# Kernel tuning notes

Measured on AMD Instinct MI355X. Metric: run time of the kernel, lower is better.

## Reference

```python
import jax, jax.numpy as jnp
import numpy as np

B, D_IN, D_H, D_OUT = 1024, 1024, 4096, 1024
SPARSITY = 0.5  # fraction of weights KEPT (top-k)


def setup_inputs() -> dict:
    key = jax.random.key(0)
    ks = jax.random.split(key, 13)
    def kaiming(k, shape):
        fan_in = shape[-1] if len(shape) > 1 else shape[0]
        bound = 1.0 / np.sqrt(fan_in)
        return jax.random.uniform(k, shape, jnp.float32, -bound, bound)
    inp = {
        "x":   jax.random.normal(ks[0], (B, D_IN), jnp.float32),
        "W1":  kaiming(ks[1], (D_H, D_IN)),
        "b1":  kaiming(ks[2], (D_H,)),
        "W2":  kaiming(ks[3], (D_H, D_H)),
        "b2":  kaiming(ks[4], (D_H,)),
        "W3":  kaiming(ks[5], (D_OUT, D_H)),
        "b3":  kaiming(ks[6], (D_OUT,)),
        # scores: kaiming-uniform for weights, N(0, 0.01) for biases (as in Mask.__init__)
        "sW1": kaiming(ks[7], (D_H, D_IN)),
        "sb1": 0.01 * jax.random.normal(ks[8], (D_H,), jnp.float32),
        "sW2": kaiming(ks[9], (D_H, D_H)),
        "sb2": 0.01 * jax.random.normal(ks[10], (D_H,), jnp.float32),
        "sW3": kaiming(ks[11], (D_OUT, D_H)),
        "sb3": 0.01 * jax.random.normal(ks[12], (D_OUT,), jnp.float32),
    }
    return inp


def _global_masks(scores):
    """Single fused global top-k threshold mask (replaces O(P) redundant sorts).
    Bottom (1-SPARSITY) fraction (by value rank) -> 0, top SPARSITY fraction -> 1."""
    flat = jnp.concatenate([s.ravel() for s in scores])
    n = flat.shape[0]
    j = int((1.0 - SPARSITY) * n)  # number of zeroed entries
    idx = jnp.argsort(flat)
    bin_mask = jnp.zeros((n,), flat.dtype).at[idx[j:]].set(1.0)
    # straight-through: d(mask)/d(score) = 1 (GetSubnet_global.backward returns g)
    st_mask = bin_mask + flat - jax.lax.stop_gradient(flat)
    sizes = [int(np.prod(s.shape)) for s in scores]
    offs = np.concatenate([[0], np.cumsum(sizes)])
    return [st_mask[offs[i]:offs[i + 1]].reshape(scores[i].shape)
            for i in range(len(scores))]


def reference(x, W1, b1, W2, b2, W3, b3, sW1, sb1, sW2, sb2, sW3, sb3):
    masks = _global_masks([sW1, sb1, sW2, sb2, sW3, sb3])
    mW1, mb1, mW2, mb2, mW3, mb3 = masks
    # masked params, then MLP forward (torch Linear: y = x @ W.T + b)
    h = jax.nn.relu(x @ (W1 * mW1).T + b1 * mb1)
    h = jax.nn.relu(h @ (W2 * mW2).T + b2 * mb2)
    return h @ (W3 * mW3).T + b3 * mb3
```

## Files before the change

### kernel.cpp

```cpp
#include <hip/hip_runtime.h>
#include <hip/hip_bf16.h>
#include <stdint.h>


typedef __bf16 bf16_t;
typedef __bf16 bf16x4 __attribute__((ext_vector_type(4)));
typedef __bf16 bf16x8 __attribute__((ext_vector_type(8)));
typedef float  f32x4  __attribute__((ext_vector_type(4)));

using gvoid = const __attribute__((address_space(1))) void;
using svoid = __attribute__((address_space(3))) void;

#define O1 4194304L
#define O2 4198400L
#define O3 20975616L
#define O4 20979712L
#define O5 25174016L
#define N_TOT 25175040L
#define J_RANK 12587520u
#define CAND_CAP 4096

#define WS_HIST 0u
#define WS_RES  32768u
#define WS_CNT  32784u
#define WS_CAND 32800u
#define WS_W1B  131072u
#define WS_B1F  8519680u
#define WS_W2B  8536064u
#define WS_B2F  42090496u
#define WS_W3B  42106880u
#define WS_B3F  50495488u
#define WS_H1F  50511872u
#define WS_H2F  58900480u
#define WS_FAST_END 67289088ull
#define WS_H1   131072u
#define WS_H2   8519680u

#define SWZ(row, chunk) ((((chunk) + ((row) >> 1)) & 3))

__device__ __forceinline__ unsigned int mono32(float f) {
    unsigned int u = __float_as_uint(f);
    return (u & 0x80000000u) ? ~u : (u | 0x80000000u);
}

__global__ __launch_bounds__(256) void zero_kernel(unsigned int* p, int n) {
    int i = blockIdx.x * 256 + threadIdx.x;
    if (i < n) p[i] = 0u;
}

__global__ __launch_bounds__(256) void cvt_x_kernel(const float* __restrict__ x,
                                                    bf16_t* __restrict__ xb, int n8) {
    int i = blockIdx.x * 256 + threadIdx.x;
    if (i < n8) {
        const float4 a = *(const float4*)(x + (size_t)i * 8);
        const float4 b = *(const float4*)(x + (size_t)i * 8 + 4);
        bf16x8 r;
        r[0] = (__bf16)a.x; r[1] = (__bf16)a.y; r[2] = (__bf16)a.z; r[3] = (__bf16)a.w;
        r[4] = (__bf16)b.x; r[5] = (__bf16)b.y; r[6] = (__bf16)b.z; r[7] = (__bf16)b.w;
        *(bf16x8*)(xb + (size_t)i * 8) = r;
    }
}

__device__ __forceinline__ void seg_lookup(long e,
    const float* s0, const float* s1, const float* s2,
    const float* s3, const float* s4, const float* s5,
    const float** sp, long* off) {
    if (e < O1)      { *sp = s0; *off = e; }
    else if (e < O2) { *sp = s1; *off = e - O1; }
    else if (e < O3) { *sp = s2; *off = e - O2; }
    else if (e < O4) { *sp = s3; *off = e - O3; }
    else if (e < O5) { *sp = s4; *off = e - O4; }
    else             { *sp = s5; *off = e - O5; }
}

__global__ __launch_bounds__(256) void hist_kernel(
    const float* s0, const float* s1, const float* s2,
    const float* s3, const float* s4, const float* s5,
    unsigned int* hist) {
    __shared__ unsigned int lh[8192];
    for (int i = threadIdx.x; i < 8192; i += 256) lh[i] = 0u;
    __syncthreads();
    const long ng = N_TOT / 4;
    for (long g = (long)blockIdx.x * 256 + threadIdx.x; g < ng;
         g += (long)gridDim.x * 256) {
        long e = g * 4;
        const float* sp; long o;
        seg_lookup(e, s0, s1, s2, s3, s4, s5, &sp, &o);
        float4 v = *(const float4*)(sp + o);
        atomicAdd(&lh[mono32(v.x) >> 19], 1u);
        atomicAdd(&lh[mono32(v.y) >> 19], 1u);
        atomicAdd(&lh[mono32(v.z) >> 19], 1u);
        atomicAdd(&lh[mono32(v.w) >> 19], 1u);
    }
    __syncthreads();
    for (int i = threadIdx.x; i < 8192; i += 256) {
        unsigned int c = lh[i];
        if (c) atomicAdd(&hist[i], c);
    }
}

__global__ __launch_bounds__(256) void select_kernel(const unsigned int* hist,
                                                     unsigned int* res) {
    __shared__ unsigned int part[256];
    int tid = threadIdx.x;
    unsigned int s = 0;
    for (int b = tid * 32; b < tid * 32 + 32; ++b) s += hist[b];
    part[tid] = s;
    __syncthreads();
    if (tid == 0) {
        unsigned int acc = 0;
        for (int i = 0; i < 256; ++i) { unsigned int v = part[i]; part[i] = acc; acc += v; }
    }
    __syncthreads();
    unsigned int acc = part[tid];
    for (int b = tid * 32; b < tid * 32 + 32; ++b) {
        unsigned int h = hist[b];
        if (acc <= J_RANK && J_RANK < acc + h) {
            res[0] = (unsigned int)b;
            res[1] = acc;
            res[2] = J_RANK - acc;
        }
        acc += h;
    }
}

__global__ __launch_bounds__(256) void mask_apply_fast(
    const float* s0, const float* s1, const float* s2,
    const float* s3, const float* s4, const float* s5,
    const float* w0, const float* w1, const float* w2,
    const float* w3, const float* w4, const float* w5,
    bf16_t* W1b, float* b1f, bf16_t* W2b, float* b2f, bf16_t* W3b, float* b3f,
    const unsigned int* res, unsigned int* cand_cnt, unsigned long long* cand) {
    const unsigned int C = res[0];
    const long ng = N_TOT / 4;
    for (long g = (long)blockIdx.x * 256 + threadIdx.x; g < ng;
         g += (long)gridDim.x * 256) {
        long e = g * 4;
        const float* sp; long o;
        seg_lookup(e, s0, s1, s2, s3, s4, s5, &sp, &o);
        const float* wp;
        if (e < O1)      wp = w0;
        else if (e < O2) wp = w1;
        else if (e < O3) wp = w2;
        else if (e < O4) wp = w3;
        else if (e < O5) wp = w4;
        else             wp = w5;
        float4 sv = *(const float4*)(sp + o);
        float4 wv = *(const float4*)(wp + o);
#define PROC(comp, ci)                                                         \
        { unsigned int key = mono32(sv.comp); unsigned int kb = key >> 19;     \
          if (kb < C) wv.comp = 0.f;                                           \
          else if (kb == C) {                                                  \
              unsigned int slot = atomicAdd(cand_cnt, 1u);                     \
              if (slot < CAND_CAP)                                             \
                  cand[slot] = (((unsigned long long)key) << 32) |             \
                               (unsigned long long)(unsigned int)(e + ci);     \
          } }
        PROC(x, 0) PROC(y, 1) PROC(z, 2) PROC(w, 3)
#undef PROC
        if (e < O1) {
            bf16x4 b; b[0]=(__bf16)wv.x; b[1]=(__bf16)wv.y; b[2]=(__bf16)wv.z; b[3]=(__bf16)wv.w;
            *(bf16x4*)(W1b + o) = b;
        } else if (e < O2) {
            *(float4*)(b1f + o) = wv;
        } else if (e < O3) {
            bf16x4 b; b[0]=(__bf16)wv.x; b[1]=(__bf16)wv.y; b[2]=(__bf16)wv.z; b[3]=(__bf16)wv.w;
            *(bf16x4*)(W2b + o) = b;
        } else if (e < O4) {
            *(float4*)(b2f + o) = wv;
        } else if (e < O5) {
            bf16x4 b; b[0]=(__bf16)wv.x; b[1]=(__bf16)wv.y; b[2]=(__bf16)wv.z; b[3]=(__bf16)wv.w;
            *(bf16x4*)(W3b + o) = b;
        } else {
            *(float4*)(b3f + o) = wv;
        }
    }
}

__global__ __launch_bounds__(256) void finalize_fast(
    const unsigned int* res, const unsigned int* cand_cnt,
    const unsigned long long* cand,
    bf16_t* W1b, float* b1f, bf16_t* W2b, float* b2f, bf16_t* W3b, float* b3f) {
    __shared__ unsigned long long buf[CAND_CAP];
    int tid = threadIdx.x;
    unsigned int cnt = *cand_cnt; if (cnt > CAND_CAP) cnt = CAND_CAP;
    unsigned int need = res[2];   if (need > cnt) need = cnt;
    for (int i = tid; i < (int)cnt; i += 256) buf[i] = cand[i];
    __syncthreads();
    for (int i = tid; i < (int)cnt; i += 256) {
        unsigned long long me = buf[i];
        unsigned int rank = 0;
        for (unsigned int j = 0; j < cnt; ++j) rank += (buf[j] < me);
        if (rank < need) {
            long idx = (long)(unsigned int)(me & 0xFFFFFFFFu);
            if (idx < O1)      W1b[idx] = (__bf16)0.f;
            else if (idx < O2) b1f[idx - O1] = 0.f;
            else if (idx < O3) W2b[idx - O2] = (__bf16)0.f;
            else if (idx < O4) b2f[idx - O3] = 0.f;
            else if (idx < O5) W3b[idx - O4] = (__bf16)0.f;
            else               b3f[idx - O5] = 0.f;
        }
    }
}

__global__ __launch_bounds__(256) void mask_apply_kernel(
    const float* s0, const float* s1, const float* s2,
    const float* s3, const float* s4, const float* s5,
    float* w0, float* w1, float* w2, float* w3, float* w4, float* w5,
    const unsigned int* res, unsigned int* cand_cnt, unsigned long long* cand) {
    const unsigned int C = res[0];
    const long ng = N_TOT / 4;
    for (long g = (long)blockIdx.x * 256 + threadIdx.x; g < ng;
         g += (long)gridDim.x * 256) {
        long e = g * 4;
        const float* sp; long o;
        seg_lookup(e, s0, s1, s2, s3, s4, s5, &sp, &o);
        float* wp;
        if (e < O1)      wp = w0;
        else if (e < O2) wp = w1;
        else if (e < O3) wp = w2;
        else if (e < O4) wp = w3;
        else if (e < O5) wp = w4;
        else             wp = w5;
        float4 sv = *(const float4*)(sp + o);
        float4 wv = *(float4*)(wp + o);
#define PROC(comp, ci)                                                         \
        { unsigned int key = mono32(sv.comp); unsigned int kb = key >> 19;     \
          if (kb < C) wv.comp = 0.f;                                           \
          else if (kb == C) {                                                  \
              unsigned int slot = atomicAdd(cand_cnt, 1u);                     \
              if (slot < CAND_CAP)                                             \
                  cand[slot] = (((unsigned long long)key) << 32) |             \
                               (unsigned long long)(unsigned int)(e + ci);     \
          } }
        PROC(x, 0) PROC(y, 1) PROC(z, 2) PROC(w, 3)
#undef PROC
        *(float4*)(wp + o) = wv;
    }
}

__global__ __launch_bounds__(256) void finalize_kernel(
    const unsigned int* res, const unsigned int* cand_cnt,
    const unsigned long long* cand,
    float* w0, float* w1, float* w2, float* w3, float* w4, float* w5) {
    __shared__ unsigned long long buf[CAND_CAP];
    int tid = threadIdx.x;
    unsigned int cnt = *cand_cnt; if (cnt > CAND_CAP) cnt = CAND_CAP;
    unsigned int need = res[2];   if (need > cnt) need = cnt;
    for (int i = tid; i < (int)cnt; i += 256) buf[i] = cand[i];
    __syncthreads();
    for (int i = tid; i < (int)cnt; i += 256) {
        unsigned long long me = buf[i];
        unsigned int rank = 0;
        for (unsigned int j = 0; j < cnt; ++j) rank += (buf[j] < me);
        if (rank < need) {
            long idx = (long)(unsigned int)(me & 0xFFFFFFFFu);
            if (idx < O1)      w0[idx] = 0.f;
            else if (idx < O2) w1[idx - O1] = 0.f;
            else if (idx < O3) w2[idx - O2] = 0.f;
            else if (idx < O4) w3[idx - O3] = 0.f;
            else if (idx < O5) w4[idx - O4] = 0.f;
            else               w5[idx - O5] = 0.f;
        }
    }
}

__device__ __forceinline__ bf16x8 load8(const float* p) {
    float4 a = *(const float4*)p;
    float4 b = *(const float4*)(p + 4);
    bf16x8 r;
    r[0] = (__bf16)a.x; r[1] = (__bf16)a.y; r[2] = (__bf16)a.z; r[3] = (__bf16)a.w;
    r[4] = (__bf16)b.x; r[5] = (__bf16)b.y; r[6] = (__bf16)b.z; r[7] = (__bf16)b.w;
    return r;
}
__device__ __forceinline__ bf16x8 load8(const bf16_t* p) {
    return *(const bf16x8*)p;
}

template <int BM, int BN, bool RELU, typename TA, typename TB, typename TC>
__global__ __launch_bounds__(256) void gemm_bt(
    const TA* __restrict__ A, const TB* __restrict__ B,
    const float* __restrict__ bias, TC* __restrict__ C,
    int M, int N, int K) {
    constexpr int BK = 32;
    constexpr int WM = BM / 2, WN = BN / 2;
    constexpr int TM = WM / 16, TN = WN / 16;
    constexpr int CA = (BM * BK) / 8;
    constexpr int CB = (BN * BK) / 8;
    __shared__ __align__(16) bf16_t As[BM * BK];
    __shared__ __align__(16) bf16_t Bs[BN * BK];

    const int tid = threadIdx.x;
    const int w = tid >> 6, lane = tid & 63;
    const int quad = lane >> 4, l16 = lane & 15;
    const int wm = (w >> 1) * WM, wn = (w & 1) * WN;
    const int rowBase = blockIdx.y * BM;
    const int colBase = blockIdx.x * BN;

    f32x4 acc[TM][TN] = {};

    const TA* Ab = A + (size_t)rowBase * K;
    const TB* Bb = B + (size_t)colBase * K;

    for (int k0 = 0; k0 < K; k0 += BK) {
        __syncthreads();
#pragma unroll
        for (int c0 = 0; c0 < CA; c0 += 256) {
            int c = c0 + tid;
            int row = c >> 2, kc = c & 3;
            *(bf16x8*)&As[row * BK + SWZ(row, kc) * 8] =
                load8(Ab + (size_t)row * K + k0 + kc * 8);
        }
#pragma unroll
        for (int c0 = 0; c0 < CB; c0 += 256) {
            int c = c0 + tid;
            int row = c >> 2, kc = c & 3;
            *(bf16x8*)&Bs[row * BK + SWZ(row, kc) * 8] =
                load8(Bb + (size_t)row * K + k0 + kc * 8);
        }
        __syncthreads();
        bf16x8 af[TM], bfr[TN];
#pragma unroll
        for (int i = 0; i < TM; ++i) {
            int r = wm + i * 16 + l16;
            af[i] = *(const bf16x8*)&As[r * BK + SWZ(r, quad) * 8];
        }
#pragma unroll
        for (int j = 0; j < TN; ++j) {
            int r = wn + j * 16 + l16;
            bfr[j] = *(const bf16x8*)&Bs[r * BK + SWZ(r, quad) * 8];
        }
#pragma unroll
        for (int i = 0; i < TM; ++i)
#pragma unroll
            for (int j = 0; j < TN; ++j)
                acc[i][j] = __builtin_amdgcn_mfma_f32_16x16x32_bf16(
                    af[i], bfr[j], acc[i][j], 0, 0, 0);
    }

#pragma unroll
    for (int i = 0; i < TM; ++i) {
#pragma unroll
        for (int j = 0; j < TN; ++j) {
            int col = colBase + wn + j * 16 + l16;
            float bv = bias[col];
#pragma unroll
            for (int r = 0; r < 4; ++r) {
                int rowg = rowBase + wm + i * 16 + quad * 4 + r;
                float v = acc[i][j][r] + bv;
                if (RELU) v = v > 0.f ? v : 0.f;
                if constexpr (sizeof(TC) == 4)
                    C[(size_t)rowg * N + col] = v;
                else
                    C[(size_t)rowg * N + col] = (bf16_t)v;
            }
        }
    }
}

template <bool RELU, int SPLITK, typename TC>
__global__ __launch_bounds__(256) void gemm_pipe(
    const bf16_t* __restrict__ A, const bf16_t* __restrict__ B,
    const float* __restrict__ bias, TC* __restrict__ C,
    int M, int N, int K) {
    constexpr int BM = 128, BN = 128, BK = 32;
    constexpr int TM = 4, TN = 4;
    constexpr int CA = (BM * BK) / 8;
    constexpr int CB = (BN * BK) / 8;
    static_assert(CA == 512 && CB == 512, "vmcnt immediates assume 4 loads/thread/step");
    __shared__ __align__(16) bf16_t As[3][BM * BK];
    __shared__ __align__(16) bf16_t Bs[3][BN * BK];

    const int tid = threadIdx.x;
    const int w = tid >> 6, lane = tid & 63;
    const int quad = lane >> 4, l16 = lane & 15;
    const int wm = (w >> 1) * 64, wn = (w & 1) * 64;
    const int rowBase = blockIdx.y * BM;
    const int colBase = blockIdx.x * BN;

    f32x4 acc[TM][TN] = {};

    const bf16_t* Ab = A + (size_t)rowBase * K;
    const bf16_t* Bb = B + (size_t)colBase * K;

    const int kPart = K / SPLITK;
    const int kBeg = (SPLITK > 1) ? (int)blockIdx.z * kPart : 0;
    const int nt = kPart / BK;

    const int rA0 = tid >> 2,        lA0 = (((tid) & 3) - (rA0 >> 1)) & 3;
    const int cH  = tid + 256;
    const int rA1 = cH >> 2,         lA1 = ((cH & 3) - (rA1 >> 1)) & 3;
    const bf16_t* aSrc0 = Ab + (size_t)rA0 * K + lA0 * 8;
    const bf16_t* aSrc1 = Ab + (size_t)rA1 * K + lA1 * 8;
    const bf16_t* bSrc0 = Bb + (size_t)rA0 * K + lA0 * 8;
    const bf16_t* bSrc1 = Bb + (size_t)rA1 * K + lA1 * 8;

    auto stage = [&](int buf, int k0) {
        __builtin_amdgcn_global_load_lds((gvoid*)(aSrc0 + k0),
            (svoid*)(As[buf] + (size_t)tid * 8), 16, 0, 0);
        __builtin_amdgcn_global_load_lds((gvoid*)(aSrc1 + k0),
            (svoid*)(As[buf] + (size_t)cH * 8), 16, 0, 0);
        __builtin_amdgcn_global_load_lds((gvoid*)(bSrc0 + k0),
            (svoid*)(Bs[buf] + (size_t)tid * 8), 16, 0, 0);
        __builtin_amdgcn_global_load_lds((gvoid*)(bSrc1 + k0),
            (svoid*)(Bs[buf] + (size_t)cH * 8), 16, 0, 0);
    };
    auto compute = [&](int buf) {
        bf16x8 af[TM], bfr[TN];
#pragma unroll
        for (int i = 0; i < TM; ++i) {
            int r = wm + i * 16 + l16;
            af[i] = *(const bf16x8*)&As[buf][r * BK + SWZ(r, quad) * 8];
        }
#pragma unroll
        for (int j = 0; j < TN; ++j) {
            int r = wn + j * 16 + l16;
            bfr[j] = *(const bf16x8*)&Bs[buf][r * BK + SWZ(r, quad) * 8];
        }
#pragma unroll
        for (int i = 0; i < TM; ++i)
#pragma unroll
            for (int j = 0; j < TN; ++j)
                acc[i][j] = __builtin_amdgcn_mfma_f32_16x16x32_bf16(
                    af[i], bfr[j], acc[i][j], 0, 0, 0);
    };

    stage(0, kBeg);
    stage(1, kBeg + BK);
    asm volatile("s_waitcnt vmcnt(4)" ::: "memory");
    __builtin_amdgcn_s_barrier();
    __builtin_amdgcn_sched_barrier(0);

    int k0 = kBeg;
    for (int t = 0; t < nt - 2; ++t, k0 += BK) {
        stage((t + 2) % 3, k0 + 2 * BK);
        compute(t % 3);
        asm volatile("s_waitcnt vmcnt(4)" ::: "memory");
        __builtin_amdgcn_s_barrier();
        __builtin_amdgcn_sched_barrier(0);
    }
    compute((nt - 2) % 3);
    asm volatile("s_waitcnt vmcnt(0)" ::: "memory");
    __builtin_amdgcn_s_barrier();
    __builtin_amdgcn_sched_barrier(0);
    compute((nt - 1) % 3);

#pragma unroll
    for (int i = 0; i < TM; ++i) {
#pragma unroll
        for (int j = 0; j < TN; ++j) {
            int col = colBase + wn + j * 16 + l16;
            float bv = (SPLITK == 1 || blockIdx.z == 0) ? bias[col] : 0.f;
#pragma unroll
            for (int r = 0; r < 4; ++r) {
                int rowg = rowBase + wm + i * 16 + quad * 4 + r;
                float v = acc[i][j][r] + bv;
                if constexpr (SPLITK == 1) {
                    if (RELU) v = v > 0.f ? v : 0.f;
                    if constexpr (sizeof(TC) == 4)
                        C[(size_t)rowg * N + col] = v;
                    else
                        C[(size_t)rowg * N + col] = (bf16_t)v;
                } else {
                    atomicAdd((float*)&C[(size_t)rowg * N + col], v);
                }
            }
        }
    }
}

extern "C" void kernel_launch(void* const* d_in, const int* in_sizes, int n_in,
                              void* d_out, int out_size, void* d_ws, size_t ws_size,
                              hipStream_t stream) {
    const float* x  = (const float*)d_in[0];
    float* W1 = (float*)d_in[1];
    float* b1 = (float*)d_in[2];
    float* W2 = (float*)d_in[3];
    float* b2 = (float*)d_in[4];
    float* W3 = (float*)d_in[5];
    float* b3 = (float*)d_in[6];
    const float* s0 = (const float*)d_in[7];
    const float* s1 = (const float*)d_in[8];
    const float* s2 = (const float*)d_in[9];
    const float* s3 = (const float*)d_in[10];
    const float* s4 = (const float*)d_in[11];
    const float* s5 = (const float*)d_in[12];

    uint8_t* ws = (uint8_t*)d_ws;
    unsigned int* hist = (unsigned int*)(ws + WS_HIST);
    unsigned int* res  = (unsigned int*)(ws + WS_RES);
    unsigned int* cnt  = (unsigned int*)(ws + WS_CNT);
    unsigned long long* cand = (unsigned long long*)(ws + WS_CAND);
    float* OUT = (float*)d_out;

    zero_kernel<<<33, 256, 0, stream>>>((unsigned int*)ws, 8200);
    hist_kernel<<<1024, 256, 0, stream>>>(s0, s1, s2, s3, s4, s5, hist);
    select_kernel<<<1, 256, 0, stream>>>(hist, res);

    if (ws_size >= WS_FAST_END) {
        bf16_t* W1b = (bf16_t*)(ws + WS_W1B);
        float*  b1f = (float*)(ws + WS_B1F);
        bf16_t* W2b = (bf16_t*)(ws + WS_W2B);
        float*  b2f = (float*)(ws + WS_B2F);
        bf16_t* W3b = (bf16_t*)(ws + WS_W3B);
        float*  b3f = (float*)(ws + WS_B3F);
        bf16_t* H1  = (bf16_t*)(ws + WS_H1F);
        bf16_t* H2  = (bf16_t*)(ws + WS_H2F);
        bf16_t* xb  = (bf16_t*)(ws + WS_H2F);
        zero_kernel<<<4096, 256, 0, stream>>>((unsigned int*)OUT, 1048576);
        cvt_x_kernel<<<512, 256, 0, stream>>>(x, xb, 131072);
        mask_apply_fast<<<2048, 256, 0, stream>>>(
            s0, s1, s2, s3, s4, s5, W1, b1, W2, b2, W3, b3,
            W1b, b1f, W2b, b2f, W3b, b3f, res, cnt, cand);
        finalize_fast<<<1, 256, 0, stream>>>(res, cnt, cand,
                                             W1b, b1f, W2b, b2f, W3b, b3f);
        gemm_pipe<true, 1, bf16_t>
            <<<dim3(32, 8), 256, 0, stream>>>(xb, W1b, b1f, H1, 1024, 4096, 1024);
        gemm_pipe<true, 1, bf16_t>
            <<<dim3(32, 8), 256, 0, stream>>>(H1, W2b, b2f, H2, 1024, 4096, 4096);
        gemm_pipe<false, 4, float>
            <<<dim3(8, 8, 4), 256, 0, stream>>>(H2, W3b, b3f, OUT, 1024, 1024, 4096);
    } else {
        bf16_t* H1 = (bf16_t*)(ws + WS_H1);
        bf16_t* H2 = (bf16_t*)(ws + WS_H2);
        mask_apply_kernel<<<2048, 256, 0, stream>>>(s0, s1, s2, s3, s4, s5,
                                                    W1, b1, W2, b2, W3, b3,
                                                    res, cnt, cand);
        finalize_kernel<<<1, 256, 0, stream>>>(res, cnt, cand,
                                               W1, b1, W2, b2, W3, b3);
        gemm_bt<64, 128, true, float, float, bf16_t>
            <<<dim3(32, 16), 256, 0, stream>>>(x, W1, b1, H1, 1024, 4096, 1024);
        gemm_bt<64, 128, true, bf16_t, float, bf16_t>
            <<<dim3(32, 16), 256, 0, stream>>>(H1, W2, b2, H2, 1024, 4096, 4096);
        gemm_bt<64, 64, false, bf16_t, float, float>
            <<<dim3(16, 16), 256, 0, stream>>>(H2, W3, b3, OUT, 1024, 1024, 4096);
    }
}
```

Baseline: 422.7 us.

## Replace histogram atomics with per-block partials and retile GEMMs with XCD swizzle

```diff
diff --git a/kernel.cpp b/kernel.cpp
--- a/kernel.cpp
+++ b/kernel.cpp
@@ -19,6 +19,8 @@
 #define N_TOT 25175040L
 #define J_RANK 12587520u
 #define CAND_CAP 4096
+
+#define HIST_BLOCKS 512
 
 #define WS_HIST 0u
 #define WS_RES  32768u
@@ -76,7 +78,7 @@
 __global__ __launch_bounds__(256) void hist_kernel(
     const float* s0, const float* s1, const float* s2,
     const float* s3, const float* s4, const float* s5,
-    unsigned int* hist) {
+    unsigned int* hb) {
     __shared__ unsigned int lh[8192];
     for (int i = threadIdx.x; i < 8192; i += 256) lh[i] = 0u;
     __syncthreads();
@@ -93,10 +95,17 @@
         atomicAdd(&lh[mono32(v.w) >> 19], 1u);
     }
     __syncthreads();
-    for (int i = threadIdx.x; i < 8192; i += 256) {
-        unsigned int c = lh[i];
-        if (c) atomicAdd(&hist[i], c);
-    }
+    unsigned int* dst = hb + (size_t)blockIdx.x * 8192;
+    for (int i = threadIdx.x; i < 8192; i += 256) dst[i] = lh[i];
+}
+
+__global__ __launch_bounds__(256) void reduce_hist(const unsigned int* __restrict__ hb,
+                                                   unsigned int* __restrict__ hist) {
+    int b = blockIdx.x * 256 + threadIdx.x;
+    unsigned int s = 0;
+    for (int blk = 0; blk < HIST_BLOCKS; ++blk)
+        s += hb[(size_t)blk * 8192 + b];
+    hist[b] = s;
 }
 
 __global__ __launch_bounds__(256) void select_kernel(const unsigned int* hist,
@@ -359,24 +368,31 @@
 }
 
 template <bool RELU, int SPLITK, typename TC>
-__global__ __launch_bounds__(256) void gemm_pipe(
+__global__ __launch_bounds__(256) void gemm2ph(
     const bf16_t* __restrict__ A, const bf16_t* __restrict__ B,
     const float* __restrict__ bias, TC* __restrict__ C,
-    int M, int N, int K) {
-    constexpr int BM = 128, BN = 128, BK = 32;
-    constexpr int TM = 4, TN = 4;
+    int M, int N, int K, int gridX) {
+    constexpr int BM = 64, BN = 128, BK = 32;
+    constexpr int TM = 2, TN = 4;
     constexpr int CA = (BM * BK) / 8;
     constexpr int CB = (BN * BK) / 8;
-    static_assert(CA == 512 && CB == 512, "vmcnt immediates assume 4 loads/thread/step");
-    __shared__ __align__(16) bf16_t As[3][BM * BK];
-    __shared__ __align__(16) bf16_t Bs[3][BN * BK];
+    static_assert(CA == 256 && CB == 512, "staging assumes 3 loads/thread/step");
+    __shared__ __align__(16) bf16_t As[2][BM * BK];
+    __shared__ __align__(16) bf16_t Bs[2][BN * BK];
 
     const int tid = threadIdx.x;
     const int w = tid >> 6, lane = tid & 63;
     const int quad = lane >> 4, l16 = lane & 15;
-    const int wm = (w >> 1) * 64, wn = (w & 1) * 64;
-    const int rowBase = blockIdx.y * BM;
-    const int colBase = blockIdx.x * BN;
+    const int wm = (w >> 1) * 32, wn = (w & 1) * 64;
+
+    const int nwg = gridX * (int)gridDim.y;
+    const int wg = (int)blockIdx.y * gridX + (int)blockIdx.x;
+    const int cpx = nwg >> 3;
+    const int swz = (wg & 7) * cpx + (wg >> 3);
+    const int bx = swz % gridX, by = swz / gridX;
+
+    const int rowBase = by * BM;
+    const int colBase = bx * BN;
 
     f32x4 acc[TM][TN] = {};
 
@@ -387,23 +403,22 @@
     const int kBeg = (SPLITK > 1) ? (int)blockIdx.z * kPart : 0;
     const int nt = kPart / BK;
 
-    const int rA0 = tid >> 2,        lA0 = (((tid) & 3) - (rA0 >> 1)) & 3;
-    const int cH  = tid + 256;
-    const int rA1 = cH >> 2,         lA1 = ((cH & 3) - (rA1 >> 1)) & 3;
-    const bf16_t* aSrc0 = Ab + (size_t)rA0 * K + lA0 * 8;
-    const bf16_t* aSrc1 = Ab + (size_t)rA1 * K + lA1 * 8;
-    const bf16_t* bSrc0 = Bb + (size_t)rA0 * K + lA0 * 8;
-    const bf16_t* bSrc1 = Bb + (size_t)rA1 * K + lA1 * 8;
+    const int rA = tid >> 2;
+    const int lA = ((tid & 3) - (rA >> 1)) & 3;
+    const int cB1 = tid + 256;
+    const int rB1 = cB1 >> 2;
+    const int lB1 = ((cB1 & 3) - (rB1 >> 1)) & 3;
+    const bf16_t* aSrc  = Ab + (size_t)rA * K + lA * 8;
+    const bf16_t* bSrc0 = Bb + (size_t)rA * K + lA * 8;
+    const bf16_t* bSrc1 = Bb + (size_t)rB1 * K + lB1 * 8;
 
     auto stage = [&](int buf, int k0) {
-        __builtin_amdgcn_global_load_lds((gvoid*)(aSrc0 + k0),
+        __builtin_amdgcn_global_load_lds((gvoid*)(aSrc + k0),
             (svoid*)(As[buf] + (size_t)tid * 8), 16, 0, 0);
-        __builtin_amdgcn_global_load_lds((gvoid*)(aSrc1 + k0),
-            (svoid*)(As[buf] + (size_t)cH * 8), 16, 0, 0);
         __builtin_amdgcn_global_load_lds((gvoid*)(bSrc0 + k0),
             (svoid*)(Bs[buf] + (size_t)tid * 8), 16, 0, 0);
         __builtin_amdgcn_global_load_lds((gvoid*)(bSrc1 + k0),
-            (svoid*)(Bs[buf] + (size_t)cH * 8), 16, 0, 0);
+            (svoid*)(Bs[buf] + (size_t)cB1 * 8), 16, 0, 0);
     };
     auto compute = [&](int buf) {
         bf16x8 af[TM], bfr[TN];
@@ -426,24 +441,13 @@
     };
 
     stage(0, kBeg);
-    stage(1, kBeg + BK);
-    asm volatile("s_waitcnt vmcnt(4)" ::: "memory");
-    __builtin_amdgcn_s_barrier();
-    __builtin_amdgcn_sched_barrier(0);
-
-    int k0 = kBeg;
-    for (int t = 0; t < nt - 2; ++t, k0 += BK) {
-        stage((t + 2) % 3, k0 + 2 * BK);
-        compute(t % 3);
-        asm volatile("s_waitcnt vmcnt(4)" ::: "memory");
-        __builtin_amdgcn_s_barrier();
-        __builtin_amdgcn_sched_barrier(0);
-    }
-    compute((nt - 2) % 3);
-    asm volatile("s_waitcnt vmcnt(0)" ::: "memory");
-    __builtin_amdgcn_s_barrier();
-    __builtin_amdgcn_sched_barrier(0);
-    compute((nt - 1) % 3);
+    __syncthreads();
+    for (int t = 0; t < nt - 1; ++t) {
+        stage((t + 1) & 1, kBeg + (t + 1) * BK);
+        compute(t & 1);
+        __syncthreads();
+    }
+    compute((nt - 1) & 1);
 
 #pragma unroll
     for (int i = 0; i < TM; ++i) {
@@ -494,8 +498,6 @@
     float* OUT = (float*)d_out;
 
     zero_kernel<<<33, 256, 0, stream>>>((unsigned int*)ws, 8200);
-    hist_kernel<<<1024, 256, 0, stream>>>(s0, s1, s2, s3, s4, s5, hist);
-    select_kernel<<<1, 256, 0, stream>>>(hist, res);
 
     if (ws_size >= WS_FAST_END) {
         bf16_t* W1b = (bf16_t*)(ws + WS_W1B);
@@ -506,7 +508,12 @@
         float*  b3f = (float*)(ws + WS_B3F);
         bf16_t* H1  = (bf16_t*)(ws + WS_H1F);
         bf16_t* H2  = (bf16_t*)(ws + WS_H2F);
+        unsigned int* hb = (unsigned int*)(ws + WS_W2B);
         bf16_t* xb  = (bf16_t*)(ws + WS_H2F);
+
+        hist_kernel<<<HIST_BLOCKS, 256, 0, stream>>>(s0, s1, s2, s3, s4, s5, hb);
+        reduce_hist<<<32, 256, 0, stream>>>(hb, hist);
+        select_kernel<<<1, 256, 0, stream>>>(hist, res);
         zero_kernel<<<4096, 256, 0, stream>>>((unsigned int*)OUT, 1048576);
         cvt_x_kernel<<<512, 256, 0, stream>>>(x, xb, 131072);
         mask_apply_fast<<<2048, 256, 0, stream>>>(
@@ -514,15 +521,17 @@
             W1b, b1f, W2b, b2f, W3b, b3f, res, cnt, cand);
         finalize_fast<<<1, 256, 0, stream>>>(res, cnt, cand,
                                              W1b, b1f, W2b, b2f, W3b, b3f);
-        gemm_pipe<true, 1, bf16_t>
-            <<<dim3(32, 8), 256, 0, stream>>>(xb, W1b, b1f, H1, 1024, 4096, 1024);
-        gemm_pipe<true, 1, bf16_t>
-            <<<dim3(32, 8), 256, 0, stream>>>(H1, W2b, b2f, H2, 1024, 4096, 4096);
-        gemm_pipe<false, 4, float>
-            <<<dim3(8, 8, 4), 256, 0, stream>>>(H2, W3b, b3f, OUT, 1024, 1024, 4096);
+        gemm2ph<true, 1, bf16_t>
+            <<<dim3(32, 16), 256, 0, stream>>>(xb, W1b, b1f, H1, 1024, 4096, 1024, 32);
+        gemm2ph<true, 1, bf16_t>
+            <<<dim3(32, 16), 256, 0, stream>>>(H1, W2b, b2f, H2, 1024, 4096, 4096, 32);
+        gemm2ph<false, 4, float>
+            <<<dim3(8, 16, 4), 256, 0, stream>>>(H2, W3b, b3f, OUT, 1024, 1024, 4096, 8);
     } else {
         bf16_t* H1 = (bf16_t*)(ws + WS_H1);
         bf16_t* H2 = (bf16_t*)(ws + WS_H2);
+        hist_kernel<<<1, 256, 0, stream>>>(s0, s1, s2, s3, s4, s5, hist);
+        select_kernel<<<1, 256, 0, stream>>>(hist, res);
         mask_apply_kernel<<<2048, 256, 0, stream>>>(s0, s1, s2, s3, s4, s5,
                                                     W1, b1, W2, b2, W3, b3,
                                                     res, cnt, cand);
```

Measured after the change: 399.4 us. 5.5% less time.
